# Performance work log

Measured on AMD Instinct MI355X. Metric: run time of the kernel, lower is better.

The kernel has to match this reference:

```python
import jax, jax.numpy as jnp
import numpy as np

N = 100000   # nodes
E = 1600000  # edges
IN = 128     # in_dim
H = 64       # h_dim
T = 20000    # treated nodes
C = 20000    # control nodes


def setup_inputs() -> dict:
    key = jax.random.key(0)
    ks = jax.random.split(key, 12)
    x = jax.random.normal(ks[0], (N, IN), dtype=jnp.float32)
    edge_index = jax.random.randint(ks[1], (2, E), 0, N)
    treat_idx = jax.random.randint(ks[2], (T,), 0, N)
    control_idx = jax.random.randint(ks[3], (C,), 0, N)

    def w(k, shape):
        fan_in = shape[0]
        return jax.random.normal(k, shape, dtype=jnp.float32) * (fan_in ** -0.5)

    W1 = w(ks[4], (IN, H)); b1 = jnp.zeros((H,), jnp.float32)
    W2 = w(ks[5], (H, H));  b2 = jnp.zeros((H,), jnp.float32)
    Wy1 = w(ks[6], (H, 1)); by1 = jnp.zeros((1,), jnp.float32)
    Wy0 = w(ks[7], (H, 1)); by0 = jnp.zeros((1,), jnp.float32)
    Wp1 = w(ks[8], (H, H)); bp1 = jnp.zeros((H,), jnp.float32)
    Wp2 = w(ks[9], (H, 2)); bp2 = jnp.zeros((2,), jnp.float32)
    return dict(x=x, edge_index=edge_index, treat_idx=treat_idx, control_idx=control_idx,
                W1=W1, b1=b1, W2=W2, b2=b2, Wy1=Wy1, by1=by1, Wy0=Wy0, by0=by0,
                Wp1=Wp1, bp1=bp1, Wp2=Wp2, bp2=bp2)


def _gcn_norm(edge_index, n):
    # PyG GCNConv default: add self-loops, symmetric D^-1/2 A D^-1/2 normalization
    loop = jnp.arange(n, dtype=edge_index.dtype)
    src = jnp.concatenate([edge_index[0], loop])
    dst = jnp.concatenate([edge_index[1], loop])
    deg = jax.ops.segment_sum(jnp.ones_like(dst, dtype=jnp.float32), dst, num_segments=n)
    dinv = jnp.where(deg > 0, deg ** -0.5, 0.0)
    norm = dinv[src] * dinv[dst]  # [E+N]
    return src, dst, norm


def _gcn_conv(x, W, b, src, dst, norm, n):
    h = x @ W                              # [N,H] transform first (small GEMM)
    msg = h[src] * norm[:, None]           # gather + scale  [E+N,H]
    out = jax.ops.segment_sum(msg, dst, num_segments=n)  # scatter-add
    return out + b


def reference(x, edge_index, treat_idx, control_idx,
              W1, b1, W2, b2, Wy1, by1, Wy0, by0, Wp1, bp1, Wp2, bp2):
    n = x.shape[0]
    src, dst, norm = _gcn_norm(edge_index, n)
    lrelu = jax.nn.leaky_relu  # default negative_slope=0.01 matches torch

    xZ1 = jax.nn.relu(_gcn_conv(x, W1, b1, src, dst, norm, n))
    # F.dropout with training=False (eval) is identity
    xZ2 = _gcn_conv(xZ1, W2, b2, src, dst, norm, n)

    xt = xZ2[treat_idx]    # [T,H]
    xc = xZ2[control_idx]  # [C,H]
    y1 = lrelu(xt @ Wy1 + by1)
    yc0 = lrelu(xt @ Wy0 + by0)
    y0 = lrelu(xc @ Wy0 + by0)
    yc1 = lrelu(xc @ Wy1 + by1)
    tprob = lrelu(lrelu(xZ2 @ Wp1 + bp1) @ Wp2 + bp2)  # [N,2]

    return (y1.squeeze(-1), yc0.squeeze(-1), y0.squeeze(-1), yc1.squeeze(-1), tprob, xZ2)
```

## Files before the change

kernel.cpp:

```cpp
#include <hip/hip_runtime.h>
#include <math.h>


#define CHUNK 16384
#define BSH 7
#define CAP 3072

typedef __attribute__((ext_vector_type(8))) _Float16 half8;
typedef __attribute__((ext_vector_type(2))) _Float16 half2v;
typedef __attribute__((ext_vector_type(4))) float f32x4;

__device__ __forceinline__ float lrelu(float x) { return x > 0.0f ? x : 0.01f * x; }

__device__ __forceinline__ float wave_sum64(float v) {
#pragma unroll
  for (int m = 32; m >= 1; m >>= 1) v += __shfl_xor(v, m, 64);
  return v;
}

__launch_bounds__(1024)
__global__ void k_bin(const int* __restrict__ src, const int* __restrict__ dst,
                      int E, int nbuck, int* __restrict__ cur,
                      unsigned int* __restrict__ pairs) {
  __shared__ int bh[1024];
  __shared__ int bb[1024];
  int t = threadIdx.x;
  for (int i = t; i < nbuck; i += 1024) bh[i] = 0;
  __syncthreads();
  int e0 = blockIdx.x * CHUNK;
  int e1 = min(e0 + CHUNK, E);
  for (int e = e0 + t; e < e1; e += 1024) atomicAdd(&bh[dst[e] >> BSH], 1);
  __syncthreads();
  for (int i = t; i < nbuck; i += 1024) {
    int c = bh[i];
    bb[i] = c ? atomicAdd(&cur[i], c) : 0;
  }
  __syncthreads();
  for (int i = t; i < nbuck; i += 1024) bh[i] = 0;
  __syncthreads();
  for (int e = e0 + t; e < e1; e += 1024) {
    int s = src[e];
    int d = dst[e];
    int b = d >> BSH;
    int p = atomicAdd(&bh[b], 1);
    pairs[(size_t)b * CAP + bb[b] + p] = (unsigned int)s | ((unsigned int)(d & 127) << 20);
  }
}

__global__ void k_sort(unsigned int* __restrict__ pairs, const int* __restrict__ cur,
                       int* __restrict__ offs, int* __restrict__ cntout,
                       float* __restrict__ dinv, int N) {
  __shared__ unsigned int seg[CAP];
  __shared__ int hist[128];
  __shared__ int loc[128];
  __shared__ int lcur[128];
  int b = blockIdx.x, t = threadIdx.x;
  int c = cur[b];
  size_t base = (size_t)b * CAP;
  for (int i = t; i < c; i += 256) seg[i] = pairs[base + i];
  if (t < 128) hist[t] = 0;
  __syncthreads();
  for (int i = t; i < c; i += 256) atomicAdd(&hist[seg[i] >> 20], 1);
  __syncthreads();
  if (t < 128) loc[t] = hist[t];
  __syncthreads();
  for (int off = 1; off < 128; off <<= 1) {
    int u = (t >= off && t < 128) ? loc[t - off] : 0;
    __syncthreads();
    if (t < 128) loc[t] += u;
    __syncthreads();
  }
  if (t < 128) {
    int ex = loc[t] - hist[t];
    lcur[t] = ex;
    int node = (b << BSH) + t;
    if (node < N) {
      offs[node] = (int)base + ex;
      cntout[node] = hist[t];
      dinv[node] = rsqrtf((float)(hist[t] + 1));
    }
  }
  __syncthreads();
  for (int i = t; i < c; i += 256) {
    unsigned int p = seg[i];
    int d = (int)(p >> 20);
    int pos = atomicAdd(&lcur[d], 1);
    pairs[base + pos] = p & 0xFFFFFu;
  }
}

template <int K, typename TIN>
__launch_bounds__(256)
__global__ void k_gemm_mfma(const TIN* __restrict__ X, const float* __restrict__ W,
                            const float* __restrict__ dinv, _Float16* __restrict__ G, int N) {
  constexpr int KST = K / 32;
  int lane = threadIdx.x & 63;
  int wv = threadIdx.x >> 6;
  int lo = lane & 15;
  int hi = lane >> 4;

  half8 bfrag[KST][4];
#pragma unroll
  for (int ks = 0; ks < KST; ks++)
#pragma unroll
    for (int ct = 0; ct < 4; ct++)
#pragma unroll
      for (int j = 0; j < 8; j++)
        bfrag[ks][ct][j] = (_Float16)W[(ks * 32 + hi * 8 + j) * 64 + ct * 16 + lo];

  int r0 = (blockIdx.x * 4 + wv) * 16;
  if (r0 >= N) return;

  f32x4 acc[4];
#pragma unroll
  for (int ct = 0; ct < 4; ct++)
#pragma unroll
    for (int j = 0; j < 4; j++) acc[ct][j] = 0.0f;

  int ar = min(r0 + lo, N - 1);
#pragma unroll
  for (int ks = 0; ks < KST; ks++) {
    const TIN* ap = X + (size_t)ar * K + ks * 32 + hi * 8;
    half8 a;
    if constexpr (sizeof(TIN) == 4) {
      const float4* p = (const float4*)ap;
      float4 u = p[0], v = p[1];
      a[0] = (_Float16)u.x; a[1] = (_Float16)u.y; a[2] = (_Float16)u.z; a[3] = (_Float16)u.w;
      a[4] = (_Float16)v.x; a[5] = (_Float16)v.y; a[6] = (_Float16)v.z; a[7] = (_Float16)v.w;
    } else {
      a = *(const half8*)ap;
    }
#pragma unroll
    for (int ct = 0; ct < 4; ct++)
      acc[ct] = __builtin_amdgcn_mfma_f32_16x16x32_f16(a, bfrag[ks][ct], acc[ct], 0, 0, 0);
  }

  float dv[4];
#pragma unroll
  for (int j = 0; j < 4; j++) dv[j] = dinv[min(r0 + hi * 4 + j, N - 1)];
#pragma unroll
  for (int j = 0; j < 4; j++) {
    int rr = r0 + hi * 4 + j;
    if (rr < N) {
#pragma unroll
      for (int ct = 0; ct < 4; ct++)
        G[(size_t)rr * 64 + ct * 16 + lo] = (_Float16)(acc[ct][j] * dv[j]);
    }
  }
}

template <typename TOUT>
__launch_bounds__(256)
__global__ void k_agg(const _Float16* __restrict__ G, const int* __restrict__ offs,
                      const int* __restrict__ count, const int* __restrict__ slot,
                      const float* __restrict__ dinv, const float* __restrict__ bias,
                      TOUT* __restrict__ Out, int N, int do_relu) {
  int lane = threadIdx.x & 63;
  int wid = (blockIdx.x * blockDim.x + threadIdx.x) >> 6;
  if (wid >= N) return;
  int r = __builtin_amdgcn_readfirstlane(wid);
  int cp = lane & 31;
  int rs = lane >> 5;
  int start = offs[r], cnt = count[r];
  const _Float16* gp = G + 2 * cp;

  float sx = 0.f, sy = 0.f;
  if (rs == 0) {
    half2v v = *(const half2v*)(gp + (size_t)r * 64);
    sx += (float)v[0]; sy += (float)v[1];
  }
  for (int j = 0; j < cnt; j += 32) {
    half2v v[16];
    bool a[16];
#pragma unroll
    for (int u = 0; u < 16; u++) {
      int idx = j + 2 * u + rs;
      a[u] = idx < cnt;
      int e = slot[start + min(idx, cnt - 1)];
      v[u] = *(const half2v*)(gp + (size_t)e * 64);
    }
#pragma unroll
    for (int u = 0; u < 16; u++) {
      if (a[u]) { sx += (float)v[u][0]; sy += (float)v[u][1]; }
    }
  }
  sx += __shfl_xor(sx, 32, 64);
  sy += __shfl_xor(sy, 32, 64);

  if (rs == 0) {
    float d = dinv[r];
    float vx = bias[2 * cp] + d * sx;
    float vy = bias[2 * cp + 1] + d * sy;
    if (do_relu) { vx = fmaxf(vx, 0.f); vy = fmaxf(vy, 0.f); }
    if constexpr (sizeof(TOUT) == 2) {
      half2v o; o[0] = (_Float16)vx; o[1] = (_Float16)vy;
      *(half2v*)((_Float16*)Out + (size_t)r * 64 + 2 * cp) = o;
    } else {
      *(float2*)((float*)Out + (size_t)r * 64 + 2 * cp) = make_float2(vx, vy);
    }
  }
}

__launch_bounds__(256)
__global__ void k_tprob_mfma(const float* __restrict__ Z, const float* __restrict__ Wp1,
                             const float* __restrict__ bp1, const float* __restrict__ Wp2,
                             const float* __restrict__ bp2, float* __restrict__ tprob, int N) {
  int lane = threadIdx.x & 63;
  int wv = threadIdx.x >> 6;
  int lo = lane & 15;
  int hi = lane >> 4;

  half8 bfrag[2][4];
#pragma unroll
  for (int ks = 0; ks < 2; ks++)
#pragma unroll
    for (int ct = 0; ct < 4; ct++)
#pragma unroll
      for (int j = 0; j < 8; j++)
        bfrag[ks][ct][j] = (_Float16)Wp1[(ks * 32 + hi * 8 + j) * 64 + ct * 16 + lo];

  int r0 = (blockIdx.x * 4 + wv) * 16;
  if (r0 >= N) return;

  f32x4 acc[4];
#pragma unroll
  for (int ct = 0; ct < 4; ct++)
#pragma unroll
    for (int j = 0; j < 4; j++) acc[ct][j] = 0.0f;

  int ar = min(r0 + lo, N - 1);
#pragma unroll
  for (int ks = 0; ks < 2; ks++) {
    const float4* p = (const float4*)(Z + (size_t)ar * 64 + ks * 32 + hi * 8);
    float4 u = p[0], v = p[1];
    half8 a;
    a[0] = (_Float16)u.x; a[1] = (_Float16)u.y; a[2] = (_Float16)u.z; a[3] = (_Float16)u.w;
    a[4] = (_Float16)v.x; a[5] = (_Float16)v.y; a[6] = (_Float16)v.z; a[7] = (_Float16)v.w;
#pragma unroll
    for (int ct = 0; ct < 4; ct++)
      acc[ct] = __builtin_amdgcn_mfma_f32_16x16x32_f16(a, bfrag[ks][ct], acc[ct], 0, 0, 0);
  }

  float w20[4], w21[4], b1v[4];
#pragma unroll
  for (int ct = 0; ct < 4; ct++) {
    int col = ct * 16 + lo;
    w20[ct] = Wp2[col * 2 + 0];
    w21[ct] = Wp2[col * 2 + 1];
    b1v[ct] = bp1[col];
  }
  float b20 = bp2[0], b21 = bp2[1];

#pragma unroll
  for (int j = 0; j < 4; j++) {
    float t0 = 0.f, t1 = 0.f;
#pragma unroll
    for (int ct = 0; ct < 4; ct++) {
      float h = lrelu(acc[ct][j] + b1v[ct]);
      t0 = fmaf(h, w20[ct], t0);
      t1 = fmaf(h, w21[ct], t1);
    }
#pragma unroll
    for (int m = 1; m <= 8; m <<= 1) {
      t0 += __shfl_xor(t0, m, 64);
      t1 += __shfl_xor(t1, m, 64);
    }
    int rr = r0 + hi * 4 + j;
    if (lo == 0 && rr < N) {
      tprob[(size_t)rr * 2 + 0] = lrelu(t0 + b20);
      tprob[(size_t)rr * 2 + 1] = lrelu(t1 + b21);
    }
  }
}

__global__ void k_heads(const float* __restrict__ Z, const int* __restrict__ treat,
                        const int* __restrict__ ctrl, int T, int C,
                        const float* __restrict__ Wy1, const float* __restrict__ by1,
                        const float* __restrict__ Wy0, const float* __restrict__ by0,
                        float* __restrict__ y1, float* __restrict__ yc0,
                        float* __restrict__ y0, float* __restrict__ yc1) {
  int lane = threadIdx.x & 63;
  int wid = (blockIdx.x * blockDim.x + threadIdx.x) >> 6;
  if (wid >= T + C) return;
  bool treated = wid < T;
  int idx = treated ? wid : wid - T;
  int row = treated ? treat[idx] : ctrl[idx];
  row = __builtin_amdgcn_readfirstlane(row);
  float v = Z[(size_t)row * 64 + lane];
  float s1 = wave_sum64(v * Wy1[lane]);
  float s0 = wave_sum64(v * Wy0[lane]);
  if (lane == 0) {
    float a1 = lrelu(s1 + by1[0]);
    float a0 = lrelu(s0 + by0[0]);
    if (treated) { y1[idx] = a1; yc0[idx] = a0; }
    else         { yc1[idx] = a1; y0[idx] = a0; }
  }
}

extern "C" void kernel_launch(void* const* d_in, const int* in_sizes, int n_in,
                              void* d_out, int out_size, void* d_ws, size_t ws_size,
                              hipStream_t stream) {
  const int IN = 128, H = 64;
  const int N = in_sizes[0] / IN;
  const int E = in_sizes[1] / 2;
  const int T = in_sizes[2];
  const int C = in_sizes[3];
  const int nbuck = (N + 127) >> BSH;
  const int nblk = (E + CHUNK - 1) / CHUNK;

  const float* x    = (const float*)d_in[0];
  const int*   ei   = (const int*)d_in[1];
  const int*   src  = ei;
  const int*   dst  = ei + E;
  const int*   trt  = (const int*)d_in[2];
  const int*   ctl  = (const int*)d_in[3];
  const float* W1   = (const float*)d_in[4];
  const float* b1   = (const float*)d_in[5];
  const float* W2   = (const float*)d_in[6];
  const float* b2   = (const float*)d_in[7];
  const float* Wy1  = (const float*)d_in[8];
  const float* by1  = (const float*)d_in[9];
  const float* Wy0  = (const float*)d_in[10];
  const float* by0  = (const float*)d_in[11];
  const float* Wp1  = (const float*)d_in[12];
  const float* bp1  = (const float*)d_in[13];
  const float* Wp2  = (const float*)d_in[14];
  const float* bp2  = (const float*)d_in[15];

  float* out   = (float*)d_out;
  float* y1    = out;
  float* yc0   = out + T;
  float* y0    = out + 2 * T;
  float* yc1   = out + 2 * T + C;
  float* tprob = out + 2 * T + 2 * C;
  float* xZ2   = out + 2 * T + 2 * C + 2 * N;

  int* cur       = (int*)d_ws;
  int* offs      = cur + 1024;
  int* cnt       = offs + N;
  float* dinv    = (float*)(cnt + N);
  unsigned int* pairs = (unsigned int*)(dinv + N);
  _Float16* g16  = (_Float16*)(pairs + (size_t)nbuck * CAP);
  _Float16* xZ1  = g16 + (size_t)N * 64;

  hipMemsetAsync(cur, 0, sizeof(int) * 1024, stream);

  k_bin<<<nblk, 1024, 0, stream>>>(src, dst, E, nbuck, cur, pairs);
  k_sort<<<nbuck, 256, 0, stream>>>(pairs, cur, offs, cnt, dinv, N);

  const int ngemm = (N + 63) / 64;
  const int nagg = (int)(((size_t)N * 64 + 255) / 256);
  int* slot = (int*)pairs;

  k_gemm_mfma<128, float><<<ngemm, 256, 0, stream>>>(x, W1, dinv, g16, N);
  k_agg<_Float16><<<nagg, 256, 0, stream>>>(g16, offs, cnt, slot, dinv, b1, xZ1, N, 1);

  k_gemm_mfma<64, _Float16><<<ngemm, 256, 0, stream>>>(xZ1, W2, dinv, g16, N);
  k_agg<float><<<nagg, 256, 0, stream>>>(g16, offs, cnt, slot, dinv, b2, xZ2, N, 0);

  k_tprob_mfma<<<ngemm, 256, 0, stream>>>(xZ2, Wp1, bp1, Wp2, bp2, tprob, N);
  k_heads<<<((size_t)(T + C) * 64 + 255) / 256, 256, 0, stream>>>(
      xZ2, trt, ctl, T, C, Wy1, by1, Wy0, by0, y1, yc0, y0, yc1);
}
```

Baseline: 190.8 us.

## Pad CSR rows to 32 with dummy zero node and merge tail kernels

```diff
diff --git a/kernel.cpp b/kernel.cpp
--- a/kernel.cpp
+++ b/kernel.cpp
@@ -2,9 +2,9 @@
 #include <math.h>
 
 
-#define CHUNK 16384
+#define CHUNK 8192
 #define BSH 7
-#define CAP 3072
+#define CAP 4608
 
 typedef __attribute__((ext_vector_type(8))) _Float16 half8;
 typedef __attribute__((ext_vector_type(2))) _Float16 half2v;
@@ -54,6 +54,7 @@
   __shared__ int hist[128];
   __shared__ int loc[128];
   __shared__ int lcur[128];
+  __shared__ int pbase[128];
   int b = blockIdx.x, t = threadIdx.x;
   int c = cur[b];
   size_t base = (size_t)b * CAP;
@@ -62,7 +63,7 @@
   __syncthreads();
   for (int i = t; i < c; i += 256) atomicAdd(&hist[seg[i] >> 20], 1);
   __syncthreads();
-  if (t < 128) loc[t] = hist[t];
+  if (t < 128) loc[t] = (hist[t] + 31) & ~31;
   __syncthreads();
   for (int off = 1; off < 128; off <<= 1) {
     int u = (t >= off && t < 128) ? loc[t - off] : 0;
@@ -71,12 +72,14 @@
     __syncthreads();
   }
   if (t < 128) {
-    int ex = loc[t] - hist[t];
-    lcur[t] = ex;
+    int r32 = (hist[t] + 31) & ~31;
+    int pex = loc[t] - r32;
+    lcur[t] = pex;
+    pbase[t] = pex;
     int node = (b << BSH) + t;
     if (node < N) {
-      offs[node] = (int)base + ex;
-      cntout[node] = hist[t];
+      offs[node] = (int)base + pex;
+      cntout[node] = r32;
       dinv[node] = rsqrtf((float)(hist[t] + 1));
     }
   }
@@ -86,6 +89,11 @@
     int d = (int)(p >> 20);
     int pos = atomicAdd(&lcur[d], 1);
     pairs[base + pos] = p & 0xFFFFFu;
+  }
+  __syncthreads();
+  if (t < 128) {
+    int r32 = (hist[t] + 31) & ~31;
+    for (int p = hist[t]; p < r32; p++) pairs[base + pbase[t] + p] = (unsigned int)N;
   }
 }
 
@@ -98,6 +106,8 @@
   int wv = threadIdx.x >> 6;
   int lo = lane & 15;
   int hi = lane >> 4;
+
+  if (blockIdx.x == 0 && threadIdx.x < 64) G[(size_t)N * 64 + threadIdx.x] = (_Float16)0.0f;
 
   half8 bfrag[KST][4];
 #pragma unroll
@@ -171,18 +181,13 @@
   }
   for (int j = 0; j < cnt; j += 32) {
     half2v v[16];
-    bool a[16];
 #pragma unroll
     for (int u = 0; u < 16; u++) {
-      int idx = j + 2 * u + rs;
-      a[u] = idx < cnt;
-      int e = slot[start + min(idx, cnt - 1)];
+      int e = slot[start + j + 2 * u + rs];
       v[u] = *(const half2v*)(gp + (size_t)e * 64);
     }
 #pragma unroll
-    for (int u = 0; u < 16; u++) {
-      if (a[u]) { sx += (float)v[u][0]; sy += (float)v[u][1]; }
-    }
+    for (int u = 0; u < 16; u++) { sx += (float)v[u][0]; sy += (float)v[u][1]; }
   }
   sx += __shfl_xor(sx, 32, 64);
   sy += __shfl_xor(sy, 32, 64);
@@ -202,98 +207,100 @@
 }
 
 __launch_bounds__(256)
-__global__ void k_tprob_mfma(const float* __restrict__ Z, const float* __restrict__ Wp1,
-                             const float* __restrict__ bp1, const float* __restrict__ Wp2,
-                             const float* __restrict__ bp2, float* __restrict__ tprob, int N) {
+__global__ void k_finish(const float* __restrict__ Z,
+                         const float* __restrict__ Wp1, const float* __restrict__ bp1,
+                         const float* __restrict__ Wp2, const float* __restrict__ bp2,
+                         float* __restrict__ tprob,
+                         const int* __restrict__ treat, const int* __restrict__ ctrl,
+                         int T, int C,
+                         const float* __restrict__ Wy1, const float* __restrict__ by1,
+                         const float* __restrict__ Wy0, const float* __restrict__ by0,
+                         float* __restrict__ y1, float* __restrict__ yc0,
+                         float* __restrict__ y0, float* __restrict__ yc1,
+                         int N, int ngemm) {
   int lane = threadIdx.x & 63;
-  int wv = threadIdx.x >> 6;
-  int lo = lane & 15;
-  int hi = lane >> 4;
-
-  half8 bfrag[2][4];
-#pragma unroll
-  for (int ks = 0; ks < 2; ks++)
+  if ((int)blockIdx.x < ngemm) {
+    int wv = threadIdx.x >> 6;
+    int lo = lane & 15;
+    int hi = lane >> 4;
+
+    half8 bfrag[2][4];
+#pragma unroll
+    for (int ks = 0; ks < 2; ks++)
+#pragma unroll
+      for (int ct = 0; ct < 4; ct++)
+#pragma unroll
+        for (int j = 0; j < 8; j++)
+          bfrag[ks][ct][j] = (_Float16)Wp1[(ks * 32 + hi * 8 + j) * 64 + ct * 16 + lo];
+
+    int r0 = (blockIdx.x * 4 + wv) * 16;
+    if (r0 >= N) return;
+
+    f32x4 acc[4];
 #pragma unroll
     for (int ct = 0; ct < 4; ct++)
 #pragma unroll
-      for (int j = 0; j < 8; j++)
-        bfrag[ks][ct][j] = (_Float16)Wp1[(ks * 32 + hi * 8 + j) * 64 + ct * 16 + lo];
-
-  int r0 = (blockIdx.x * 4 + wv) * 16;
-  if (r0 >= N) return;
-
-  f32x4 acc[4];
-#pragma unroll
-  for (int ct = 0; ct < 4; ct++)
-#pragma unroll
-    for (int j = 0; j < 4; j++) acc[ct][j] = 0.0f;
-
-  int ar = min(r0 + lo, N - 1);
-#pragma unroll
-  for (int ks = 0; ks < 2; ks++) {
-    const float4* p = (const float4*)(Z + (size_t)ar * 64 + ks * 32 + hi * 8);
-    float4 u = p[0], v = p[1];
-    half8 a;
-    a[0] = (_Float16)u.x; a[1] = (_Float16)u.y; a[2] = (_Float16)u.z; a[3] = (_Float16)u.w;
-    a[4] = (_Float16)v.x; a[5] = (_Float16)v.y; a[6] = (_Float16)v.z; a[7] = (_Float16)v.w;
-#pragma unroll
-    for (int ct = 0; ct < 4; ct++)
-      acc[ct] = __builtin_amdgcn_mfma_f32_16x16x32_f16(a, bfrag[ks][ct], acc[ct], 0, 0, 0);
-  }
-
-  float w20[4], w21[4], b1v[4];
-#pragma unroll
-  for (int ct = 0; ct < 4; ct++) {
-    int col = ct * 16 + lo;
-    w20[ct] = Wp2[col * 2 + 0];
-    w21[ct] = Wp2[col * 2 + 1];
-    b1v[ct] = bp1[col];
-  }
-  float b20 = bp2[0], b21 = bp2[1];
-
-#pragma unroll
-  for (int j = 0; j < 4; j++) {
-    float t0 = 0.f, t1 = 0.f;
+      for (int j = 0; j < 4; j++) acc[ct][j] = 0.0f;
+
+    int ar = min(r0 + lo, N - 1);
+#pragma unroll
+    for (int ks = 0; ks < 2; ks++) {
+      const float4* p = (const float4*)(Z + (size_t)ar * 64 + ks * 32 + hi * 8);
+      float4 u = p[0], v = p[1];
+      half8 a;
+      a[0] = (_Float16)u.x; a[1] = (_Float16)u.y; a[2] = (_Float16)u.z; a[3] = (_Float16)u.w;
+      a[4] = (_Float16)v.x; a[5] = (_Float16)v.y; a[6] = (_Float16)v.z; a[7] = (_Float16)v.w;
+#pragma unroll
+      for (int ct = 0; ct < 4; ct++)
+        acc[ct] = __builtin_amdgcn_mfma_f32_16x16x32_f16(a, bfrag[ks][ct], acc[ct], 0, 0, 0);
+    }
+
+    float w20[4], w21[4], b1v[4];
 #pragma unroll
     for (int ct = 0; ct < 4; ct++) {
-      float h = lrelu(acc[ct][j] + b1v[ct]);
-      t0 = fmaf(h, w20[ct], t0);
-      t1 = fmaf(h, w21[ct], t1);
-    }
-#pragma unroll
-    for (int m = 1; m <= 8; m <<= 1) {
-      t0 += __shfl_xor(t0, m, 64);
-      t1 += __shfl_xor(t1, m, 64);
-    }
-    int rr = r0 + hi * 4 + j;
-    if (lo == 0 && rr < N) {
-      tprob[(size_t)rr * 2 + 0] = lrelu(t0 + b20);
-      tprob[(size_t)rr * 2 + 1] = lrelu(t1 + b21);
-    }
-  }
-}
-
-__global__ void k_heads(const float* __restrict__ Z, const int* __restrict__ treat,
-                        const int* __restrict__ ctrl, int T, int C,
-                        const float* __restrict__ Wy1, const float* __restrict__ by1,
-                        const float* __restrict__ Wy0, const float* __restrict__ by0,
-                        float* __restrict__ y1, float* __restrict__ yc0,
-                        float* __restrict__ y0, float* __restrict__ yc1) {
-  int lane = threadIdx.x & 63;
-  int wid = (blockIdx.x * blockDim.x + threadIdx.x) >> 6;
-  if (wid >= T + C) return;
-  bool treated = wid < T;
-  int idx = treated ? wid : wid - T;
-  int row = treated ? treat[idx] : ctrl[idx];
-  row = __builtin_amdgcn_readfirstlane(row);
-  float v = Z[(size_t)row * 64 + lane];
-  float s1 = wave_sum64(v * Wy1[lane]);
-  float s0 = wave_sum64(v * Wy0[lane]);
-  if (lane == 0) {
-    float a1 = lrelu(s1 + by1[0]);
-    float a0 = lrelu(s0 + by0[0]);
-    if (treated) { y1[idx] = a1; yc0[idx] = a0; }
-    else         { yc1[idx] = a1; y0[idx] = a0; }
+      int col = ct * 16 + lo;
+      w20[ct] = Wp2[col * 2 + 0];
+      w21[ct] = Wp2[col * 2 + 1];
+      b1v[ct] = bp1[col];
+    }
+    float b20 = bp2[0], b21 = bp2[1];
+
+#pragma unroll
+    for (int j = 0; j < 4; j++) {
+      float t0 = 0.f, t1 = 0.f;
+#pragma unroll
+      for (int ct = 0; ct < 4; ct++) {
+        float h = lrelu(acc[ct][j] + b1v[ct]);
+        t0 = fmaf(h, w20[ct], t0);
+        t1 = fmaf(h, w21[ct], t1);
+      }
+#pragma unroll
+      for (int m = 1; m <= 8; m <<= 1) {
+        t0 += __shfl_xor(t0, m, 64);
+        t1 += __shfl_xor(t1, m, 64);
+      }
+      int rr = r0 + hi * 4 + j;
+      if (lo == 0 && rr < N) {
+        tprob[(size_t)rr * 2 + 0] = lrelu(t0 + b20);
+        tprob[(size_t)rr * 2 + 1] = lrelu(t1 + b21);
+      }
+    }
+  } else {
+    int wid = (((int)blockIdx.x - ngemm) * (int)blockDim.x + (int)threadIdx.x) >> 6;
+    if (wid >= T + C) return;
+    bool treated = wid < T;
+    int idx = treated ? wid : wid - T;
+    int row = treated ? treat[idx] : ctrl[idx];
+    row = __builtin_amdgcn_readfirstlane(row);
+    float v = Z[(size_t)row * 64 + lane];
+    float s1 = wave_sum64(v * Wy1[lane]);
+    float s0 = wave_sum64(v * Wy0[lane]);
+    if (lane == 0) {
+      float a1 = lrelu(s1 + by1[0]);
+      float a0 = lrelu(s0 + by0[0]);
+      if (treated) { y1[idx] = a1; yc0[idx] = a0; }
+      else         { yc1[idx] = a1; y0[idx] = a0; }
+    }
   }
 }
 
@@ -341,7 +348,7 @@
   float* dinv    = (float*)(cnt + N);
   unsigned int* pairs = (unsigned int*)(dinv + N);
   _Float16* g16  = (_Float16*)(pairs + (size_t)nbuck * CAP);
-  _Float16* xZ1  = g16 + (size_t)N * 64;
+  _Float16* xZ1  = g16 + (size_t)(N + 1) * 64;
 
   hipMemsetAsync(cur, 0, sizeof(int) * 1024, stream);
 
@@ -350,6 +357,7 @@
 
   const int ngemm = (N + 63) / 64;
   const int nagg = (int)(((size_t)N * 64 + 255) / 256);
+  const int nheads = (int)(((size_t)(T + C) * 64 + 255) / 256);
   int* slot = (int*)pairs;
 
   k_gemm_mfma<128, float><<<ngemm, 256, 0, stream>>>(x, W1, dinv, g16, N);
@@ -358,7 +366,7 @@
   k_gemm_mfma<64, _Float16><<<ngemm, 256, 0, stream>>>(xZ1, W2, dinv, g16, N);
   k_agg<float><<<nagg, 256, 0, stream>>>(g16, offs, cnt, slot, dinv, b2, xZ2, N, 0);
 
-  k_tprob_mfma<<<ngemm, 256, 0, stream>>>(xZ2, Wp1, bp1, Wp2, bp2, tprob, N);
-  k_heads<<<((size_t)(T + C) * 64 + 255) / 256, 256, 0, stream>>>(
-      xZ2, trt, ctl, T, C, Wy1, by1, Wy0, by0, y1, yc0, y0, yc1);
-}
+  k_finish<<<ngemm + nheads, 256, 0, stream>>>(
+      xZ2, Wp1, bp1, Wp2, bp2, tprob, trt, ctl, T, C,
+      Wy1, by1, Wy0, by0, y1, yc0, y0, yc1, N, ngemm);
+}
```

New measurement: 174.5 us. 8.5% less time.
